# Performance work log

Hardware: AMD Instinct MI355X
Metric: run time of the kernel (lower is better)

## Reference

```python
import jax, jax.numpy as jnp
import numpy as np

EPS = 1e-15
MAXN = 1.0 - 1e-5  # projection radius for c=1 Poincare ball

def _norm(x):
    return jnp.sqrt(jnp.clip(jnp.sum(x * x, axis=-1, keepdims=True), EPS))

def _artanh(x):
    return jnp.arctanh(jnp.clip(x, -1.0 + 1e-7, 1.0 - 1e-7))

def projx(x):
    n = _norm(x)
    return jnp.where(n > MAXN, x * (MAXN / n), x)

def expmap0(v):
    n = _norm(v)
    return jnp.tanh(n) * v / n

def logmap0(x):
    n = _norm(x)
    return _artanh(n) * x / n

def mobius_add(x, y):
    x2 = jnp.sum(x * x, -1, keepdims=True)
    y2 = jnp.sum(y * y, -1, keepdims=True)
    xy = jnp.sum(x * y, -1, keepdims=True)
    num = (1.0 + 2.0 * xy + y2) * x + (1.0 - x2) * y
    den = 1.0 + 2.0 * xy + x2 * y2
    return num / jnp.clip(den, EPS)

def _lam(x):
    return 2.0 / jnp.clip(1.0 - jnp.sum(x * x, -1, keepdims=True), EPS)

def expmap(x, v):
    n = _norm(v)
    second = jnp.tanh(_lam(x) * n / 2.0) * v / n
    return projx(mobius_add(x, second))

def logmap(x, y):
    u = mobius_add(-x, y)
    n = _norm(u)
    return (2.0 / _lam(x)) * _artanh(n) * u / n

def mobius_matvec(W, x):
    mx = x @ W.T
    xn = _norm(x)
    mxn = _norm(mx)
    return jnp.tanh(mxn / xn * _artanh(xn)) * mx / mxn

def setup_inputs() -> dict:
    key = jax.random.key(0)
    ks = jax.random.split(key, 8)
    B, L, F = 128, 336, 128
    SEG, D, H, T = 24, 128, 256, 8
    return {
        "x": jax.random.normal(ks[0], (B, L, F), jnp.float32),
        "revin_w": jnp.ones((F,), jnp.float32),
        "revin_b": jnp.zeros((F,), jnp.float32),
        "W_enc": jax.random.normal(ks[1], (SEG, D), jnp.float32) * 0.05,
        "b_enc": jax.random.normal(ks[2], (D,), jnp.float32) * 0.01,
        "W_vel": jax.random.normal(ks[3], (D, D), jnp.float32) * (1.0 / np.sqrt(D)),
        "b_vel": jax.random.normal(ks[4], (D,), jnp.float32) * 0.01,
        "step_sizes": jnp.array(1.0, jnp.float32),
        "W1": jax.random.normal(ks[5], (D, H), jnp.float32) * (1.0 / np.sqrt(D)),
        "b1": jnp.zeros((H,), jnp.float32),
        "W2": jax.random.normal(ks[6], (H, SEG), jnp.float32) * (1.0 / np.sqrt(H)),
        "b2": jnp.zeros((SEG,), jnp.float32),
    }

def reference(x, revin_w, revin_b, W_enc, b_enc, W_vel, b_vel, step_sizes, W1, b1, W2, b2):
    B, L, F = x.shape
    SEG = W_enc.shape[0]
    D = W_enc.shape[1]
    N = L // SEG            # 14 history segments
    T = 192 // SEG          # 8 prediction segments
    # RevIN norm (per-series stats over time)
    mu = jnp.mean(x, axis=1, keepdims=True)            # [B,1,F]
    std = jnp.sqrt(jnp.var(x, axis=1, keepdims=True) + 1e-5)
    xn = (x - mu) / std * revin_w + revin_b
    # channel-independent: [B*F, N, SEG]
    xb = xn.transpose(0, 2, 1).reshape(B * F, N, SEG)
    # segment encoder -> Poincare ball
    z = projx(expmap0(xb @ W_enc + b_enc))             # [BF,N,D]
    # initial velocity from discounted logmap differences
    vels = logmap(z[:, :-1, :], z[:, 1:, :])           # [BF,N-1,D]
    w = 0.9 ** (N - 2 - jnp.arange(N - 1, dtype=x.dtype))
    w = w / jnp.sum(w)
    v_init = jnp.mean(vels * w[None, :, None], axis=1)  # [BF,D]
    z0 = z[:, -1, :]
    # PoincareLinear velocity net: mobius matvec + bias point + projection
    v0t = projx(mobius_add(mobius_matvec(W_vel, v_init), expmap0(b_vel)))
    step = jax.nn.sigmoid(step_sizes)
    t_vals = jnp.arange(1, T + 1, dtype=x.dtype)
    v_all = step * t_vals[None, :, None] * v0t[:, None, :]  # [BF,T,D]
    z_fut = expmap(z0[:, None, :], v_all)                   # [BF,T,D]
    # shared reconstruction head in tangent space at origin
    tan = logmap0(z_fut)
    h = jax.nn.relu(tan @ W1 + b1)
    out = h @ W2 + b2                                       # [BF,T,SEG]
    pred = out.reshape(B, F, T * SEG).transpose(0, 2, 1)    # [B,pred_len,F]
    # RevIN denorm
    pred = (pred - revin_b) / revin_w * std + mu
    return pred
```

## Files before the change

### kernel.cpp

```cpp
#include <hip/hip_runtime.h>
#include <hip/hip_bf16.h>

#define EPSF 1e-15f
#define MAXNF 0.99999f

typedef __attribute__((ext_vector_type(8))) short short8v;
typedef __attribute__((ext_vector_type(8))) ushort ushort8v;
typedef __attribute__((ext_vector_type(4))) float f32x4;

__device__ __forceinline__ float wave_sum(float v) {
#pragma unroll
    for (int off = 32; off > 0; off >>= 1) v += __shfl_xor(v, off, 64);
    return v;
}
__device__ __forceinline__ float rcpf(float x) { return __builtin_amdgcn_rcpf(x); }
__device__ __forceinline__ float tanh_g(float x) {
    if (x < 0.03f) return x * (1.f - 0.33333333f * x * x);
    float e = __expf(-2.f * x);
    return (1.f - e) * rcpf(1.f + e);
}
__device__ __forceinline__ float atanh_g(float x) {
    if (x < 0.03f) return x * (1.f + 0.33333333f * x * x);
    return 0.5f * __logf((1.f + x) * rcpf(1.f - x));
}
__device__ __forceinline__ float tanh_b(float x) {
    float e = __expf(-2.f * x);
    float tv = (1.f - e) * rcpf(1.f + e);
    float sv = x * (1.f - 0.33333333f * x * x);
    return (x < 0.03f) ? sv : tv;
}
__device__ __forceinline__ float atanh_b(float x) {
    float lv = 0.5f * __logf((1.f + x) * rcpf(1.f - x));
    float sv = x * (1.f + 0.33333333f * x * x);
    return (x < 0.03f) ? sv : lv;
}
__device__ __forceinline__ ushort f2bf(float f) {
    uint32_t u = __float_as_uint(f);
    uint32_t r = (u + 0x7fffu + ((u >> 16) & 1u)) >> 16;
    return (ushort)r;
}
__device__ __forceinline__ float bf2f(ushort u) { return __uint_as_float(((uint32_t)u) << 16); }

__global__ __launch_bounds__(256) void k_prep(
    const float* __restrict__ W1, const float* __restrict__ W2,
    const float* __restrict__ W_vel, const float* __restrict__ b_vel,
    const float* __restrict__ W_enc, const float* __restrict__ b_enc,
    ushort* __restrict__ W1t, ushort* __restrict__ W2tp,
    ushort* __restrict__ WB25h, ushort* __restrict__ WB25l,
    ushort* __restrict__ MB25h, ushort* __restrict__ MB25l,
    float* __restrict__ gq,
    float* __restrict__ cvec, float* __restrict__ scp) {
    int bid = blockIdx.x, tid = threadIdx.x;
    if (bid == 0) {
        __shared__ float red[4];
        float v = (tid < 128) ? b_vel[tid] : 0.f;
        float p = wave_sum(v * v);
        if ((tid & 63) == 0) red[tid >> 6] = p;
        __syncthreads();
        float ssq = red[0] + red[1] + red[2] + red[3];
        float nn = sqrtf(fmaxf(ssq, EPSF));
        float th = tanhf(nn);
        if (tid < 128) cvec[tid] = th / nn * v;
        if (tid == 0) scp[0] = th * th;
    } else if (bid <= 128) {
        int idx = (bid - 1) * 256 + tid;
        int n = idx >> 7, k = idx & 127;
        W1t[idx] = f2bf(W1[k * 256 + n]);
    } else if (bid <= 160) {
        int idx = (bid - 129) * 256 + tid;
        int s = idx >> 8, j = idx & 255;
        W2tp[idx] = (s < 24) ? f2bf(W2[j * 24 + s]) : (ushort)0;
    } else if (bid <= 176) {
        int idx = (bid - 161) * 256 + tid;
        int d = idx >> 5, s = idx & 31;
        float val = (s < 24) ? W_enc[s * 128 + d] : (s == 24 ? b_enc[d] : 0.f);
        ushort h = f2bf(val);
        WB25h[idx] = h;
        WB25l[idx] = f2bf(val - bf2f(h));
    } else if (bid <= 327) {
        int o = (bid - 177) * 4 + (tid >> 6);
        int lane = tid & 63;
        if (o < 601) {
            const float* pa; const float* pb;
            if (o < 576)      { pa = W_enc + (o / 24) * 128; pb = W_enc + (o % 24) * 128; }
            else if (o < 600) { pa = W_enc + (o - 576) * 128; pb = b_enc; }
            else              { pa = b_enc; pb = b_enc; }
            float2 a = *(const float2*)(pa + lane * 2);
            float2 c = *(const float2*)(pb + lane * 2);
            float p = wave_sum(a.x * c.x + a.y * c.y);
            if (lane == 0) gq[o] = p;
        }
    } else {
        int j = (bid - 328) * 4 + (tid >> 6);
        int lane = tid & 63;
        float2 wv = *(const float2*)(W_vel + j * 128 + lane * 2);
        for (int s = 0; s < 25; ++s) {
            const float* pa = (s < 24) ? (W_enc + s * 128) : b_enc;
            float2 a = *(const float2*)(pa + lane * 2);
            float p = wave_sum(wv.x * a.x + wv.y * a.y);
            if (lane == 0) {
                ushort h = f2bf(p);
                MB25h[j * 32 + s] = h;
                MB25l[j * 32 + s] = f2bf(p - bf2f(h));
            }
        }
        if (lane >= 25 && lane < 32) { MB25h[j * 32 + lane] = 0; MB25l[j * 32 + lane] = 0; }
    }
}

__global__ __launch_bounds__(256) void k_stats(
    const float* __restrict__ x, const float* __restrict__ revin_w, const float* __restrict__ revin_b,
    float* __restrict__ sc_o, float* __restrict__ sh_o,
    float* __restrict__ osc_o, float* __restrict__ osh_o) {
    __shared__ float ps[8][32], ps2[8][32];
    int b = blockIdx.x >> 2, fg = blockIdx.x & 3, tid = threadIdx.x;
    int f = fg * 32 + (tid & 31), sl = tid >> 5;
    const float* xp = x + ((size_t)b * 336 + sl * 42) * 128 + f;
    float s = 0.f, s2 = 0.f;
    for (int l = 0; l < 42; ++l) { float v = xp[(size_t)l * 128]; s += v; s2 += v * v; }
    ps[sl][tid & 31] = s; ps2[sl][tid & 31] = s2;
    __syncthreads();
    if (tid < 32) {
        float S = 0.f, S2 = 0.f;
#pragma unroll
        for (int h = 0; h < 8; ++h) { S += ps[h][tid]; S2 += ps2[h][tid]; }
        float m = S * (1.f / 336.f);
        float var = S2 * (1.f / 336.f) - m * m;
        float sd = sqrtf(var + 1e-5f);
        int ff = fg * 32 + tid;
        int r = b * 128 + ff;
        float rw = revin_w[ff], rb = revin_b[ff];
        float sc = rw * rcpf(sd);
        sc_o[r] = sc;
        sh_o[r] = rb - m * sc;
        float oc = sd * rcpf(rw);
        osc_o[r] = oc;
        osh_o[r] = m - rb * oc;
    }
}

__global__ __launch_bounds__(256) void k_gram(
    const float* __restrict__ x, const float* __restrict__ sc_i, const float* __restrict__ sh_i,
    const float* __restrict__ gq, ushort* __restrict__ Avz) {
    __shared__ float xall[336 * 33];
    __shared__ float scs[32], shs[32];
    int bidx = blockIdx.x;
    int b = bidx >> 2, f0 = (bidx & 3) * 32;
    int tid = threadIdx.x;
    if (tid < 32) { scs[tid] = sc_i[b * 128 + f0 + tid]; shs[tid] = sh_i[b * 128 + f0 + tid]; }
    __syncthreads();
    for (int e = tid; e < 336 * 32; e += 256) {
        int l = e >> 5, fi = e & 31;
        xall[l * 33 + fi] = x[((size_t)b * 336 + l) * 128 + f0 + fi] * scs[fi] + shs[fi];
    }
    int lane = tid & 63, w = tid >> 6;
    int f = w * 8 + (lane >> 3), p = lane & 7;
    int t0 = 3 * p;
    float Greg[3][24], wbr[3];
#pragma unroll
    for (int i = 0; i < 3; ++i) {
#pragma unroll
        for (int s = 0; s < 24; ++s) Greg[i][s] = gq[(t0 + i) * 24 + s];
        wbr[i] = gq[576 + t0 + i];
    }
    float bb = gq[600];
    __syncthreads();

    float wsum = 0.f; { float pp = 1.f; for (int k2 = 0; k2 < 13; ++k2) { wsum += pp; pp *= 0.9f; } }
    float wi; { float pp = 1.f; for (int k2 = 0; k2 < 12; ++k2) pp *= 0.9f; wi = pp / (wsum * 13.f); }
    float c[14];
#pragma unroll
    for (int m = 0; m < 14; ++m) c[m] = 0.f;
    float sczp = 0.f, szp = 0.f, pwprev = 0.f;
    float xp0 = 0.f, xp1 = 0.f, xp2 = 0.f;
#pragma unroll
    for (int n = 0; n < 14; ++n) {
        float g0 = 0.f, g1 = 0.f, g2 = 0.f;
#pragma unroll
        for (int s = 0; s < 24; ++s) {
            float xv = xall[(n * 24 + s) * 33 + f];
            g0 += Greg[0][s] * xv; g1 += Greg[1][s] * xv; g2 += Greg[2][s] * xv;
        }
        float xm0 = xall[(n * 24 + t0) * 33 + f];
        float xm1 = xall[(n * 24 + t0 + 1) * 33 + f];
        float xm2 = xall[(n * 24 + t0 + 2) * 33 + f];
        float pd1 = g0 * xm0 + g1 * xm1 + g2 * xm2;
        float pw  = wbr[0] * xm0 + wbr[1] * xm1 + wbr[2] * xm2;
        float pd2 = g0 * xp0 + g1 * xp1 + g2 * xp2;
#pragma unroll
        for (int off = 1; off < 8; off <<= 1) {
            pd1 += __shfl_xor(pd1, off, 64);
            pd2 += __shfl_xor(pd2, off, 64);
            pw  += __shfl_xor(pw, off, 64);
        }
        float ssq = pd1 + 2.f * pw + bb;
        float nn = sqrtf(fmaxf(ssq, EPSF));
        float th = tanh_g(nn);
        float scz, sz;
        if (th > MAXNF) { scz = MAXNF * rcpf(nn); sz = MAXNF * MAXNF; }
        else            { scz = th * rcpf(nn);    sz = th * th; }
        if (n > 0) {
            float dotup = pd2 + pwprev + pw + bb;
            float xyp = sczp * scz * dotup;
            float t2 = 1.f - 2.f * xyp;
            float den = fmaxf(t2 + szp * sz, EPSF);
            float rden = rcpf(den);
            float a1 = t2 + sz, a2 = 1.f - szp;
            float usq = (a1 * a1 * szp - 2.f * a1 * a2 * xyp + a2 * a2 * sz) * (rden * rden);
            float un = sqrtf(fmaxf(usq, EPSF));
            float art = atanh_g(fminf(un, 1.f - 1e-7f));
            float fac = fmaxf(a2, EPSF) * art * rcpf(un) * rden * wi;
            c[n - 1] += -fac * a1 * sczp;
            c[n]     +=  fac * a2 * scz;
            wi *= (1.f / 0.9f);
        }
        sczp = scz; szp = sz; pwprev = pw;
        xp0 = xm0; xp1 = xm1; xp2 = xm2;
    }
    float s_v = 0.f;
#pragma unroll
    for (int m = 0; m < 14; ++m) s_v += c[m];
    float scz = sczp;
    size_t rbase = ((size_t)(b * 128 + f0 + f)) * 128;
#pragma unroll
    for (int q = 0; q < 4; ++q) {
        int u = 4 * p + q;
        float vv, vz;
        if (u < 24) {
            float acc = 0.f;
#pragma unroll
            for (int n = 0; n < 14; ++n) acc += c[n] * xall[(n * 24 + u) * 33 + f];
            vv = acc;
            vz = scz * xall[(312 + u) * 33 + f];
        } else if (u == 24) { vv = s_v; vz = scz; }
        else { vv = 0.f; vz = 0.f; }
        ushort vh = f2bf(vv); ushort vl = f2bf(vv - bf2f(vh));
        ushort zh = f2bf(vz); ushort zl = f2bf(vz - bf2f(zh));
        Avz[rbase + u] = vh;
        Avz[rbase + 32 + u] = vl;
        Avz[rbase + 64 + u] = zh;
        Avz[rbase + 96 + u] = zl;
    }
}

__global__ __launch_bounds__(256) void k_vz(
    const ushort* __restrict__ Avz,
    const ushort* __restrict__ WB25h, const ushort* __restrict__ WB25l,
    const ushort* __restrict__ MB25h, const ushort* __restrict__ MB25l,
    float* __restrict__ vinit_o, float* __restrict__ z0_o, float* __restrict__ mx_o) {
    int tid = threadIdx.x;
    int wid = tid >> 6, lane = tid & 63;
    int lrow = lane & 15, lk = lane >> 4;
    int r0 = blockIdx.x * 64;
    short8v BWh[2], BWl[2], BMh[2], BMl[2];
#pragma unroll
    for (int dt = 0; dt < 2; ++dt) {
        int d = wid * 32 + dt * 16 + lrow;
        BWh[dt] = *(const short8v*)(WB25h + d * 32 + lk * 8);
        BWl[dt] = *(const short8v*)(WB25l + d * 32 + lk * 8);
        BMh[dt] = *(const short8v*)(MB25h + d * 32 + lk * 8);
        BMl[dt] = *(const short8v*)(MB25l + d * 32 + lk * 8);
    }
#pragma unroll
    for (int rg = 0; rg < 4; ++rg) {
        const ushort* ap = Avz + (size_t)(r0 + rg * 16 + lrow) * 128;
        short8v Avh = *(const short8v*)(ap + lk * 8);
        short8v Avl = *(const short8v*)(ap + 32 + lk * 8);
        short8v Azh = *(const short8v*)(ap + 64 + lk * 8);
        short8v Azl = *(const short8v*)(ap + 96 + lk * 8);
#pragma unroll
        for (int dt = 0; dt < 2; ++dt) {
            f32x4 aV = (f32x4)(0.f), aZ = (f32x4)(0.f), aM = (f32x4)(0.f);
            aV = __builtin_amdgcn_mfma_f32_16x16x32_bf16(Avh, BWh[dt], aV, 0, 0, 0);
            aV = __builtin_amdgcn_mfma_f32_16x16x32_bf16(Avh, BWl[dt], aV, 0, 0, 0);
            aV = __builtin_amdgcn_mfma_f32_16x16x32_bf16(Avl, BWh[dt], aV, 0, 0, 0);
            aZ = __builtin_amdgcn_mfma_f32_16x16x32_bf16(Azh, BWh[dt], aZ, 0, 0, 0);
            aZ = __builtin_amdgcn_mfma_f32_16x16x32_bf16(Azh, BWl[dt], aZ, 0, 0, 0);
            aZ = __builtin_amdgcn_mfma_f32_16x16x32_bf16(Azl, BWh[dt], aZ, 0, 0, 0);
            aM = __builtin_amdgcn_mfma_f32_16x16x32_bf16(Avh, BMh[dt], aM, 0, 0, 0);
            aM = __builtin_amdgcn_mfma_f32_16x16x32_bf16(Avh, BMl[dt], aM, 0, 0, 0);
            aM = __builtin_amdgcn_mfma_f32_16x16x32_bf16(Avl, BMh[dt], aM, 0, 0, 0);
            int d = wid * 32 + dt * 16 + lrow;
#pragma unroll
            for (int j = 0; j < 4; ++j) {
                size_t rr = (size_t)(r0 + rg * 16 + lk * 4 + j) * 128 + d;
                vinit_o[rr] = aV[j];
                z0_o[rr] = aZ[j];
                mx_o[rr] = aM[j];
            }
        }
    }
}

__global__ __launch_bounds__(256) void k_future(
    const float* __restrict__ z0_i, const float* __restrict__ vinit, const float* __restrict__ mx_i,
    const float* __restrict__ cvec, const float* __restrict__ scp,
    const float* __restrict__ step_sizes, ushort* __restrict__ tanb) {
    int wid = threadIdx.x >> 6, lane = threadIdx.x & 63;
    int r = blockIdx.x * 4 + wid;
    size_t base = (size_t)r * 128 + lane * 2;
    float2 vi = *(const float2*)&vinit[base];
    float2 mx = *(const float2*)&mx_i[base];
    float2 z0 = *(const float2*)&z0_i[base];
    float2 cv = *(const float2*)&cvec[lane * 2];
    float scc = scp[0];
    float xn2  = wave_sum(vi.x * vi.x + vi.y * vi.y);
    float mxn2 = wave_sum(mx.x * mx.x + mx.y * mx.y);
    float mxc  = wave_sum(mx.x * cv.x + mx.y * cv.y);
    float z0mx = wave_sum(z0.x * mx.x + z0.y * mx.y);
    float z0c  = wave_sum(z0.x * cv.x + z0.y * cv.y);
    float x2   = wave_sum(z0.x * z0.x + z0.y * z0.y);
    float xn = sqrtf(fmaxf(xn2, EPSF));
    float mxn = sqrtf(fmaxf(mxn2, EPSF));
    float artx = atanh_g(fminf(xn, 1.f - 1e-7f));
    float tm = tanh_g(mxn * rcpf(xn) * artx);
    float scm = tm * rcpf(mxn);
    float sm = tm * tm;
    float xy2 = scm * mxc;
    float den2 = fmaxf(1.f + 2.f * xy2 + sm * scc, EPSF);
    float rd2 = rcpf(den2);
    float A2 = (1.f + 2.f * xy2 + scc) * scm * rd2;
    float B2 = (1.f - sm) * rd2;
    float v0n2 = A2 * A2 * mxn2 + 2.f * A2 * B2 * mxc + B2 * B2 * scc;
    float nv0 = sqrtf(fmaxf(v0n2, EPSF));
    if (nv0 > MAXNF) { float pf = MAXNF * rcpf(nv0); A2 *= pf; B2 *= pf; nv0 = MAXNF; }
    v0n2 = nv0 * nv0;
    float inv_nv0 = rcpf(nv0);
    float zdv = A2 * z0mx + B2 * z0c;
    float v00 = A2 * mx.x + B2 * cv.x, v01 = A2 * mx.y + B2 * cv.y;
    float il = rcpf(fmaxf(1.f - x2, EPSF));
    float step = rcpf(1.f + __expf(-step_sizes[0]));
    float tl = (float)((lane & 7) + 1);
    float nt_ = step * tl * nv0;
    float th = tanh_b(nt_ * il);
    float xy = th * inv_nv0 * zdv;
    float y2 = th * th;
    float den = fmaxf(1.f + 2.f * xy + x2 * y2, EPSF);
    float rd = rcpf(den);
    float A = (1.f + 2.f * xy + y2) * rd;
    float B = (1.f - x2) * th * inv_nv0 * rd;
    float rsq = A * A * x2 + 2.f * A * B * zdv + B * B * v0n2;
    float nr = sqrtf(fmaxf(rsq, EPSF));
    float pf2 = (nr > MAXNF) ? MAXNF * rcpf(nr) : 1.f;
    A *= pf2; B *= pf2; nr = fminf(nr, MAXNF);
    float art = atanh_b(fminf(nr, 1.f - 1e-7f));
    float tf = art * rcpf(nr);
    float FA = tf * A, FB = tf * B;
    uint* t32 = (uint*)tanb;
    int bb = r >> 7, f = r & 127;
#pragma unroll
    for (int t = 0; t < 8; ++t) {
        float FAt = __shfl(FA, t);
        float FBt = __shfl(FB, t);
        uint pk = (uint)f2bf(FAt * z0.x + FBt * v00) | ((uint)f2bf(FAt * z0.y + FBt * v01) << 16);
        t32[((size_t)(bb * 1024 + t * 128 + f)) * 64 + lane] = pk;
    }
}

__global__ __launch_bounds__(256, 2) void k_head(
    const ushort* __restrict__ tanb, const ushort* __restrict__ W1t, const float* __restrict__ b1,
    const ushort* __restrict__ W2tp, const float* __restrict__ b2,
    const float* __restrict__ osc_i, const float* __restrict__ osh_i,
    float* __restrict__ out) {
    __shared__ __align__(16) ushort hs[64][264];
    int tid = threadIdx.x;
    int wid = tid >> 6, lane = tid & 63;
    int lrow = lane & 15, lk = lane >> 4;

    short8v Bw[4][4];
#pragma unroll
    for (int nt = 0; nt < 4; ++nt) {
        const ushort* wp = W1t + (size_t)((wid * 4 + nt) * 16 + lrow) * 128 + lk * 8;
#pragma unroll
        for (int kk = 0; kk < 4; ++kk) Bw[nt][kk] = *(const short8v*)(wp + kk * 32);
    }
    float b1v[4];
#pragma unroll
    for (int nt = 0; nt < 4; ++nt) b1v[nt] = b1[(wid * 4 + nt) * 16 + lrow];
    float b2a = (lrow < 24) ? b2[lrow] : 0.f;
    float b2bv = (lrow < 8) ? b2[16 + lrow] : 0.f;

    int tile0 = blockIdx.x * 4;
    int bbk = tile0 >> 4;
    int fr = wid * 16 + lk * 4;
    f32x4 oc0 = *(const f32x4*)&osc_i[bbk * 128 + fr];
    f32x4 oh0 = *(const f32x4*)&osh_i[bbk * 128 + fr];
    f32x4 oc1 = *(const f32x4*)&osc_i[bbk * 128 + 64 + fr];
    f32x4 oh1 = *(const f32x4*)&osh_i[bbk * 128 + 64 + fr];

    short8v A[4][4];
    {
        const ushort* tp = tanb + ((size_t)tile0 * 64 + lrow) * 128 + lk * 8;
#pragma unroll
        for (int rg = 0; rg < 4; ++rg)
#pragma unroll
            for (int kk = 0; kk < 4; ++kk)
                A[rg][kk] = *(const short8v*)(tp + (size_t)rg * 2048 + kk * 32);
    }
#pragma unroll
    for (int it = 0; it < 4; ++it) {
        int tile = tile0 + it;
        f32x4 acc[4][4];
#pragma unroll
        for (int rg = 0; rg < 4; ++rg)
#pragma unroll
            for (int nt = 0; nt < 4; ++nt) acc[rg][nt] = (f32x4)(0.f);
#pragma unroll
        for (int kk = 0; kk < 4; ++kk)
#pragma unroll
            for (int rg = 0; rg < 4; ++rg)
#pragma unroll
                for (int nt = 0; nt < 4; ++nt)
                    acc[rg][nt] = __builtin_amdgcn_mfma_f32_16x16x32_bf16(A[rg][kk], Bw[nt][kk], acc[rg][nt], 0, 0, 0);
        if (it + 1 < 4) {
            const ushort* tp = tanb + ((size_t)(tile + 1) * 64 + lrow) * 128 + lk * 8;
#pragma unroll
            for (int rg = 0; rg < 4; ++rg)
#pragma unroll
                for (int kk = 0; kk < 4; ++kk)
                    A[rg][kk] = *(const short8v*)(tp + (size_t)rg * 2048 + kk * 32);
        }
        __syncthreads();
#pragma unroll
        for (int rg = 0; rg < 4; ++rg)
#pragma unroll
            for (int nt = 0; nt < 4; ++nt)
#pragma unroll
                for (int j = 0; j < 4; ++j)
                    hs[rg * 16 + lk * 4 + j][(wid * 4 + nt) * 16 + lrow] =
                        f2bf(fmaxf(acc[rg][nt][j] + b1v[nt], 0.f));
        __syncthreads();
        f32x4 acc2[2];
        acc2[0] = (f32x4)(0.f); acc2[1] = (f32x4)(0.f);
#pragma unroll
        for (int kk2 = 0; kk2 < 8; ++kk2) {
            short8v Ah = *(const short8v*)&hs[wid * 16 + lrow][kk2 * 32 + lk * 8];
#pragma unroll
            for (int nt2 = 0; nt2 < 2; ++nt2) {
                short8v Bv = *(const short8v*)(W2tp + (size_t)(nt2 * 16 + lrow) * 256 + kk2 * 32 + lk * 8);
                acc2[nt2] = __builtin_amdgcn_mfma_f32_16x16x32_bf16(Ah, Bv, acc2[nt2], 0, 0, 0);
            }
        }
        int rem = tile & 15, tt = rem >> 1, fhalf = rem & 1;
        f32x4 oc = fhalf ? oc1 : oc0;
        f32x4 oh = fhalf ? oh1 : oh0;
        int f0 = fhalf << 6;
#pragma unroll
        for (int nt2 = 0; nt2 < 2; ++nt2) {
            int col = nt2 * 16 + lrow;
            if (col < 24) {
                float bb2 = (nt2 == 0) ? b2a : b2bv;
                f32x4 v = acc2[nt2];
                v[0] = (v[0] + bb2) * oc[0] + oh[0];
                v[1] = (v[1] + bb2) * oc[1] + oh[1];
                v[2] = (v[2] + bb2) * oc[2] + oh[2];
                v[3] = (v[3] + bb2) * oc[3] + oh[3];
                *(f32x4*)&out[((size_t)bbk * 192 + tt * 24 + col) * 128 + f0 + fr] = v;
            }
        }
    }
}

extern "C" void kernel_launch(void* const* d_in, const int* in_sizes, int n_in,
                              void* d_out, int out_size, void* d_ws, size_t ws_size,
                              hipStream_t stream) {
    (void)in_sizes; (void)n_in; (void)out_size; (void)ws_size;
    const float* x          = (const float*)d_in[0];
    const float* revin_w    = (const float*)d_in[1];
    const float* revin_b    = (const float*)d_in[2];
    const float* W_enc      = (const float*)d_in[3];
    const float* b_enc      = (const float*)d_in[4];
    const float* W_vel      = (const float*)d_in[5];
    const float* b_vel      = (const float*)d_in[6];
    const float* step_sizes = (const float*)d_in[7];
    const float* W1         = (const float*)d_in[8];
    const float* b1         = (const float*)d_in[9];
    const float* W2         = (const float*)d_in[10];
    const float* b2         = (const float*)d_in[11];
    float* out = (float*)d_out;

    float* wsf   = (float*)d_ws;
    float* sc    = wsf;
    float* sh    = sc + 16384;
    float* osc   = sh + 16384;
    float* osh   = osc + 16384;
    float* z0    = osh + 16384;
    float* vinit = z0 + (size_t)16384 * 128;
    float* mx    = vinit + (size_t)16384 * 128;
    float* cvec  = mx + (size_t)16384 * 128;
    float* scp   = cvec + 128;
    float* gq    = scp + 64;
    ushort* W1t   = (ushort*)(gq + 640);
    ushort* W2tp  = W1t + 32768;
    ushort* WB25h = W2tp + 8192;
    ushort* WB25l = WB25h + 4096;
    ushort* MB25h = WB25l + 4096;
    ushort* MB25l = MB25h + 4096;
    ushort* Avz   = MB25l + 4096;
    ushort* tanb  = Avz + (size_t)16384 * 128;

    k_prep<<<dim3(360), dim3(256), 0, stream>>>(W1, W2, W_vel, b_vel, W_enc, b_enc,
                                                W1t, W2tp, WB25h, WB25l, MB25h, MB25l,
                                                gq, cvec, scp);
    k_stats<<<dim3(512), dim3(256), 0, stream>>>(x, revin_w, revin_b, sc, sh, osc, osh);
    k_gram<<<dim3(512), dim3(256), 0, stream>>>(x, sc, sh, gq, Avz);
    k_vz<<<dim3(256), dim3(256), 0, stream>>>(Avz, WB25h, WB25l, MB25h, MB25l, vinit, z0, mx);
    k_future<<<dim3(4096), dim3(256), 0, stream>>>(z0, vinit, mx, cvec, scp, step_sizes, tanb);
    k_head<<<dim3(512), dim3(256), 0, stream>>>(tanb, W1t, b1, W2tp, b2, osc, osh, out);
}
```

Baseline: 98.93 us.

## Fuse stats into gram kernel, fuse vz with future, rebalance head grid

Folds the RevIN statistics pass into the gram kernel so x is read once into shared memory and normalized in place. It also merges the vz MFMA kernel with the future-trajectory kernel, keeping z0, vinit and mx in shared memory instead of writing and re-reading three 16384x128 fp32 arrays. The head kernel now processes 2 tiles per block with double the grid. The cost is extra shared memory and larger fused kernels, which could lower occupancy.

```diff
diff --git a/kernel.cpp b/kernel.cpp
--- a/kernel.cpp
+++ b/kernel.cpp
@@ -108,17 +108,26 @@
     }
 }
 
-__global__ __launch_bounds__(256) void k_stats(
-    const float* __restrict__ x, const float* __restrict__ revin_w, const float* __restrict__ revin_b,
-    float* __restrict__ sc_o, float* __restrict__ sh_o,
+__global__ __launch_bounds__(256) void k_gram(
+    const float* __restrict__ x,
+    const float* __restrict__ revin_w, const float* __restrict__ revin_b,
+    const float* __restrict__ gq, ushort* __restrict__ Avz,
     float* __restrict__ osc_o, float* __restrict__ osh_o) {
+    __shared__ float xall[336 * 33];
     __shared__ float ps[8][32], ps2[8][32];
-    int b = blockIdx.x >> 2, fg = blockIdx.x & 3, tid = threadIdx.x;
-    int f = fg * 32 + (tid & 31), sl = tid >> 5;
-    const float* xp = x + ((size_t)b * 336 + sl * 42) * 128 + f;
+    __shared__ float scs[32], shs[32];
+    int bidx = blockIdx.x;
+    int b = bidx >> 2, f0 = (bidx & 3) * 32;
+    int tid = threadIdx.x;
+    int fi = tid & 31, g = tid >> 5;
     float s = 0.f, s2 = 0.f;
-    for (int l = 0; l < 42; ++l) { float v = xp[(size_t)l * 128]; s += v; s2 += v * v; }
-    ps[sl][tid & 31] = s; ps2[sl][tid & 31] = s2;
+    for (int k = 0; k < 42; ++k) {
+        int l = g + 8 * k;
+        float v = x[((size_t)b * 336 + l) * 128 + f0 + fi];
+        xall[l * 33 + fi] = v;
+        s += v; s2 += v * v;
+    }
+    ps[g][fi] = s; ps2[g][fi] = s2;
     __syncthreads();
     if (tid < 32) {
         float S = 0.f, S2 = 0.f;
@@ -127,31 +136,22 @@
         float m = S * (1.f / 336.f);
         float var = S2 * (1.f / 336.f) - m * m;
         float sd = sqrtf(var + 1e-5f);
-        int ff = fg * 32 + tid;
-        int r = b * 128 + ff;
+        int ff = f0 + tid;
         float rw = revin_w[ff], rb = revin_b[ff];
         float sc = rw * rcpf(sd);
-        sc_o[r] = sc;
-        sh_o[r] = rb - m * sc;
-        float oc = sd * rcpf(rw);
-        osc_o[r] = oc;
-        osh_o[r] = m - rb * oc;
-    }
-}
-
-__global__ __launch_bounds__(256) void k_gram(
-    const float* __restrict__ x, const float* __restrict__ sc_i, const float* __restrict__ sh_i,
-    const float* __restrict__ gq, ushort* __restrict__ Avz) {
-    __shared__ float xall[336 * 33];
-    __shared__ float scs[32], shs[32];
-    int bidx = blockIdx.x;
-    int b = bidx >> 2, f0 = (bidx & 3) * 32;
-    int tid = threadIdx.x;
-    if (tid < 32) { scs[tid] = sc_i[b * 128 + f0 + tid]; shs[tid] = sh_i[b * 128 + f0 + tid]; }
+        scs[tid] = sc;
+        shs[tid] = rb - m * sc;
+        float ocv = sd * rcpf(rw);
+        osc_o[b * 128 + ff] = ocv;
+        osh_o[b * 128 + ff] = m - rb * ocv;
+    }
     __syncthreads();
-    for (int e = tid; e < 336 * 32; e += 256) {
-        int l = e >> 5, fi = e & 31;
-        xall[l * 33 + fi] = x[((size_t)b * 336 + l) * 128 + f0 + fi] * scs[fi] + shs[fi];
+    {
+        float sc = scs[fi], sh = shs[fi];
+        for (int k = 0; k < 42; ++k) {
+            int l = g + 8 * k;
+            xall[l * 33 + fi] = xall[l * 33 + fi] * sc + sh;
+        }
     }
     int lane = tid & 63, w = tid >> 6;
     int f = w * 8 + (lane >> 3), p = lane & 7;
@@ -160,7 +160,7 @@
 #pragma unroll
     for (int i = 0; i < 3; ++i) {
 #pragma unroll
-        for (int s = 0; s < 24; ++s) Greg[i][s] = gq[(t0 + i) * 24 + s];
+        for (int s3 = 0; s3 < 24; ++s3) Greg[i][s3] = gq[(t0 + i) * 24 + s3];
         wbr[i] = gq[576 + t0 + i];
     }
     float bb = gq[600];
@@ -177,9 +177,9 @@
     for (int n = 0; n < 14; ++n) {
         float g0 = 0.f, g1 = 0.f, g2 = 0.f;
 #pragma unroll
-        for (int s = 0; s < 24; ++s) {
-            float xv = xall[(n * 24 + s) * 33 + f];
-            g0 += Greg[0][s] * xv; g1 += Greg[1][s] * xv; g2 += Greg[2][s] * xv;
+        for (int s3 = 0; s3 < 24; ++s3) {
+            float xv = xall[(n * 24 + s3) * 33 + f];
+            g0 += Greg[0][s3] * xv; g1 += Greg[1][s3] * xv; g2 += Greg[2][s3] * xv;
         }
         float xm0 = xall[(n * 24 + t0) * 33 + f];
         float xm1 = xall[(n * 24 + t0 + 1) * 33 + f];
@@ -243,15 +243,17 @@
     }
 }
 
-__global__ __launch_bounds__(256) void k_vz(
+__global__ __launch_bounds__(256) void k_vzfut(
     const ushort* __restrict__ Avz,
     const ushort* __restrict__ WB25h, const ushort* __restrict__ WB25l,
     const ushort* __restrict__ MB25h, const ushort* __restrict__ MB25l,
-    float* __restrict__ vinit_o, float* __restrict__ z0_o, float* __restrict__ mx_o) {
+    const float* __restrict__ cvec, const float* __restrict__ scp,
+    const float* __restrict__ step_sizes, ushort* __restrict__ tanb) {
+    __shared__ float zs[32][132], vs[32][132], ms[32][132];
     int tid = threadIdx.x;
     int wid = tid >> 6, lane = tid & 63;
     int lrow = lane & 15, lk = lane >> 4;
-    int r0 = blockIdx.x * 64;
+    int r0 = blockIdx.x * 32;
     short8v BWh[2], BWl[2], BMh[2], BMl[2];
 #pragma unroll
     for (int dt = 0; dt < 2; ++dt) {
@@ -262,7 +264,7 @@
         BMl[dt] = *(const short8v*)(MB25l + d * 32 + lk * 8);
     }
 #pragma unroll
-    for (int rg = 0; rg < 4; ++rg) {
+    for (int rg = 0; rg < 2; ++rg) {
         const ushort* ap = Avz + (size_t)(r0 + rg * 16 + lrow) * 128;
         short8v Avh = *(const short8v*)(ap + lk * 8);
         short8v Avl = *(const short8v*)(ap + 32 + lk * 8);
@@ -283,77 +285,73 @@
             int d = wid * 32 + dt * 16 + lrow;
 #pragma unroll
             for (int j = 0; j < 4; ++j) {
-                size_t rr = (size_t)(r0 + rg * 16 + lk * 4 + j) * 128 + d;
-                vinit_o[rr] = aV[j];
-                z0_o[rr] = aZ[j];
-                mx_o[rr] = aM[j];
+                int row = rg * 16 + lk * 4 + j;
+                vs[row][d] = aV[j];
+                zs[row][d] = aZ[j];
+                ms[row][d] = aM[j];
             }
         }
     }
-}
-
-__global__ __launch_bounds__(256) void k_future(
-    const float* __restrict__ z0_i, const float* __restrict__ vinit, const float* __restrict__ mx_i,
-    const float* __restrict__ cvec, const float* __restrict__ scp,
-    const float* __restrict__ step_sizes, ushort* __restrict__ tanb) {
-    int wid = threadIdx.x >> 6, lane = threadIdx.x & 63;
-    int r = blockIdx.x * 4 + wid;
-    size_t base = (size_t)r * 128 + lane * 2;
-    float2 vi = *(const float2*)&vinit[base];
-    float2 mx = *(const float2*)&mx_i[base];
-    float2 z0 = *(const float2*)&z0_i[base];
+    __syncthreads();
+    float scc = scp[0];
+    float step = rcpf(1.f + __expf(-step_sizes[0]));
     float2 cv = *(const float2*)&cvec[lane * 2];
-    float scc = scp[0];
-    float xn2  = wave_sum(vi.x * vi.x + vi.y * vi.y);
-    float mxn2 = wave_sum(mx.x * mx.x + mx.y * mx.y);
-    float mxc  = wave_sum(mx.x * cv.x + mx.y * cv.y);
-    float z0mx = wave_sum(z0.x * mx.x + z0.y * mx.y);
-    float z0c  = wave_sum(z0.x * cv.x + z0.y * cv.y);
-    float x2   = wave_sum(z0.x * z0.x + z0.y * z0.y);
-    float xn = sqrtf(fmaxf(xn2, EPSF));
-    float mxn = sqrtf(fmaxf(mxn2, EPSF));
-    float artx = atanh_g(fminf(xn, 1.f - 1e-7f));
-    float tm = tanh_g(mxn * rcpf(xn) * artx);
-    float scm = tm * rcpf(mxn);
-    float sm = tm * tm;
-    float xy2 = scm * mxc;
-    float den2 = fmaxf(1.f + 2.f * xy2 + sm * scc, EPSF);
-    float rd2 = rcpf(den2);
-    float A2 = (1.f + 2.f * xy2 + scc) * scm * rd2;
-    float B2 = (1.f - sm) * rd2;
-    float v0n2 = A2 * A2 * mxn2 + 2.f * A2 * B2 * mxc + B2 * B2 * scc;
-    float nv0 = sqrtf(fmaxf(v0n2, EPSF));
-    if (nv0 > MAXNF) { float pf = MAXNF * rcpf(nv0); A2 *= pf; B2 *= pf; nv0 = MAXNF; }
-    v0n2 = nv0 * nv0;
-    float inv_nv0 = rcpf(nv0);
-    float zdv = A2 * z0mx + B2 * z0c;
-    float v00 = A2 * mx.x + B2 * cv.x, v01 = A2 * mx.y + B2 * cv.y;
-    float il = rcpf(fmaxf(1.f - x2, EPSF));
-    float step = rcpf(1.f + __expf(-step_sizes[0]));
     float tl = (float)((lane & 7) + 1);
-    float nt_ = step * tl * nv0;
-    float th = tanh_b(nt_ * il);
-    float xy = th * inv_nv0 * zdv;
-    float y2 = th * th;
-    float den = fmaxf(1.f + 2.f * xy + x2 * y2, EPSF);
-    float rd = rcpf(den);
-    float A = (1.f + 2.f * xy + y2) * rd;
-    float B = (1.f - x2) * th * inv_nv0 * rd;
-    float rsq = A * A * x2 + 2.f * A * B * zdv + B * B * v0n2;
-    float nr = sqrtf(fmaxf(rsq, EPSF));
-    float pf2 = (nr > MAXNF) ? MAXNF * rcpf(nr) : 1.f;
-    A *= pf2; B *= pf2; nr = fminf(nr, MAXNF);
-    float art = atanh_b(fminf(nr, 1.f - 1e-7f));
-    float tf = art * rcpf(nr);
-    float FA = tf * A, FB = tf * B;
     uint* t32 = (uint*)tanb;
-    int bb = r >> 7, f = r & 127;
-#pragma unroll
-    for (int t = 0; t < 8; ++t) {
-        float FAt = __shfl(FA, t);
-        float FBt = __shfl(FB, t);
-        uint pk = (uint)f2bf(FAt * z0.x + FBt * v00) | ((uint)f2bf(FAt * z0.y + FBt * v01) << 16);
-        t32[((size_t)(bb * 1024 + t * 128 + f)) * 64 + lane] = pk;
+    for (int q = 0; q < 8; ++q) {
+        int rl = wid * 8 + q;
+        int r = r0 + rl;
+        float2 vi = *(const float2*)&vs[rl][lane * 2];
+        float2 mx = *(const float2*)&ms[rl][lane * 2];
+        float2 z0 = *(const float2*)&zs[rl][lane * 2];
+        float xn2  = wave_sum(vi.x * vi.x + vi.y * vi.y);
+        float mxn2 = wave_sum(mx.x * mx.x + mx.y * mx.y);
+        float mxc  = wave_sum(mx.x * cv.x + mx.y * cv.y);
+        float z0mx = wave_sum(z0.x * mx.x + z0.y * mx.y);
+        float z0c  = wave_sum(z0.x * cv.x + z0.y * cv.y);
+        float x2   = wave_sum(z0.x * z0.x + z0.y * z0.y);
+        float xn = sqrtf(fmaxf(xn2, EPSF));
+        float mxn = sqrtf(fmaxf(mxn2, EPSF));
+        float artx = atanh_g(fminf(xn, 1.f - 1e-7f));
+        float tm = tanh_g(mxn * rcpf(xn) * artx);
+        float scm = tm * rcpf(mxn);
+        float sm = tm * tm;
+        float xy2 = scm * mxc;
+        float den2 = fmaxf(1.f + 2.f * xy2 + sm * scc, EPSF);
+        float rd2 = rcpf(den2);
+        float A2 = (1.f + 2.f * xy2 + scc) * scm * rd2;
+        float B2 = (1.f - sm) * rd2;
+        float v0n2 = A2 * A2 * mxn2 + 2.f * A2 * B2 * mxc + B2 * B2 * scc;
+        float nv0 = sqrtf(fmaxf(v0n2, EPSF));
+        if (nv0 > MAXNF) { float pf = MAXNF * rcpf(nv0); A2 *= pf; B2 *= pf; nv0 = MAXNF; }
+        v0n2 = nv0 * nv0;
+        float inv_nv0 = rcpf(nv0);
+        float zdv = A2 * z0mx + B2 * z0c;
+        float v00 = A2 * mx.x + B2 * cv.x, v01 = A2 * mx.y + B2 * cv.y;
+        float il = rcpf(fmaxf(1.f - x2, EPSF));
+        float nt_ = step * tl * nv0;
+        float th = tanh_b(nt_ * il);
+        float xy = th * inv_nv0 * zdv;
+        float y2 = th * th;
+        float den = fmaxf(1.f + 2.f * xy + x2 * y2, EPSF);
+        float rd = rcpf(den);
+        float A = (1.f + 2.f * xy + y2) * rd;
+        float B = (1.f - x2) * th * inv_nv0 * rd;
+        float rsq = A * A * x2 + 2.f * A * B * zdv + B * B * v0n2;
+        float nr = sqrtf(fmaxf(rsq, EPSF));
+        float pf2 = (nr > MAXNF) ? MAXNF * rcpf(nr) : 1.f;
+        A *= pf2; B *= pf2; nr = fminf(nr, MAXNF);
+        float art = atanh_b(fminf(nr, 1.f - 1e-7f));
+        float tf = art * rcpf(nr);
+        float FA = tf * A, FB = tf * B;
+        int bbv = r >> 7, f = r & 127;
+#pragma unroll
+        for (int t = 0; t < 8; ++t) {
+            float FAt = __shfl(FA, t);
+            float FBt = __shfl(FB, t);
+            uint pk = (uint)f2bf(FAt * z0.x + FBt * v00) | ((uint)f2bf(FAt * z0.y + FBt * v01) << 16);
+            t32[((size_t)(bbv * 1024 + t * 128 + f)) * 64 + lane] = pk;
+        }
     }
 }
 
@@ -380,7 +378,7 @@
     float b2a = (lrow < 24) ? b2[lrow] : 0.f;
     float b2bv = (lrow < 8) ? b2[16 + lrow] : 0.f;
 
-    int tile0 = blockIdx.x * 4;
+    int tile0 = blockIdx.x * 2;
     int bbk = tile0 >> 4;
     int fr = wid * 16 + lk * 4;
     f32x4 oc0 = *(const f32x4*)&osc_i[bbk * 128 + fr];
@@ -398,7 +396,7 @@
                 A[rg][kk] = *(const short8v*)(tp + (size_t)rg * 2048 + kk * 32);
     }
 #pragma unroll
-    for (int it = 0; it < 4; ++it) {
+    for (int it = 0; it < 2; ++it) {
         int tile = tile0 + it;
         f32x4 acc[4][4];
 #pragma unroll
@@ -412,7 +410,7 @@
 #pragma unroll
                 for (int nt = 0; nt < 4; ++nt)
                     acc[rg][nt] = __builtin_amdgcn_mfma_f32_16x16x32_bf16(A[rg][kk], Bw[nt][kk], acc[rg][nt], 0, 0, 0);
-        if (it + 1 < 4) {
+        if (it + 1 < 2) {
             const ushort* tp = tanb + ((size_t)(tile + 1) * 64 + lrow) * 128 + lk * 8;
 #pragma unroll
             for (int rg = 0; rg < 4; ++rg)
@@ -480,14 +478,9 @@
     float* out = (float*)d_out;
 
     float* wsf   = (float*)d_ws;
-    float* sc    = wsf;
-    float* sh    = sc + 16384;
-    float* osc   = sh + 16384;
+    float* osc   = wsf;
     float* osh   = osc + 16384;
-    float* z0    = osh + 16384;
-    float* vinit = z0 + (size_t)16384 * 128;
-    float* mx    = vinit + (size_t)16384 * 128;
-    float* cvec  = mx + (size_t)16384 * 128;
+    float* cvec  = osh + 16384;
     float* scp   = cvec + 128;
     float* gq    = scp + 64;
     ushort* W1t   = (ushort*)(gq + 640);
@@ -502,9 +495,8 @@
     k_prep<<<dim3(360), dim3(256), 0, stream>>>(W1, W2, W_vel, b_vel, W_enc, b_enc,
                                                 W1t, W2tp, WB25h, WB25l, MB25h, MB25l,
                                                 gq, cvec, scp);
-    k_stats<<<dim3(512), dim3(256), 0, stream>>>(x, revin_w, revin_b, sc, sh, osc, osh);
-    k_gram<<<dim3(512), dim3(256), 0, stream>>>(x, sc, sh, gq, Avz);
-    k_vz<<<dim3(256), dim3(256), 0, stream>>>(Avz, WB25h, WB25l, MB25h, MB25l, vinit, z0, mx);
-    k_future<<<dim3(4096), dim3(256), 0, stream>>>(z0, vinit, mx, cvec, scp, step_sizes, tanb);
-    k_head<<<dim3(512), dim3(256), 0, stream>>>(tanb, W1t, b1, W2tp, b2, osc, osh, out);
-}
+    k_gram<<<dim3(512), dim3(256), 0, stream>>>(x, revin_w, revin_b, gq, Avz, osc, osh);
+    k_vzfut<<<dim3(512), dim3(256), 0, stream>>>(Avz, WB25h, WB25l, MB25h, MB25l,
+                                                 cvec, scp, step_sizes, tanb);
+    k_head<<<dim3(1024), dim3(256), 0, stream>>>(tanb, W1t, b1, W2tp, b2, osc, osh, out);
+}
```

Measured after the change: 99.03 us. Within noise of the previous version (+0.1%).
